# Optimization experiments

Hardware: AMD Instinct MI355X
Metric: run time of the kernel (lower is better)

## Reference

```python
import jax, jax.numpy as jnp
import numpy as np
import math

B, S, D, H, DFF = 4, 1024, 1024, 16, 4096
DH = D // H
ALPHA = 1.0
NEG = -1e20
EPS = 1e-5


def layernorm(x, g, b):
    mu = jnp.mean(x, axis=-1, keepdims=True)
    var = jnp.mean((x - mu) ** 2, axis=-1, keepdims=True)
    return (x - mu) * jax.lax.rsqrt(var + EPS) * g + b


def setup_inputs() -> dict:
    key = jax.random.key(0)
    ks = jax.random.split(key, 16)
    sc = 1.0 / math.sqrt(D)
    inp = {
        "x": jax.random.normal(ks[0], (B, S, D), jnp.float32),
        "mask": jnp.ones((B, 1, S), jnp.float32),
        "Wq": jax.random.normal(ks[1], (D, D), jnp.float32) * sc,
        "Wk": jax.random.normal(ks[2], (D, D), jnp.float32) * sc,
        "Wv": jax.random.normal(ks[3], (D, D), jnp.float32) * sc,
        "ln1_g": jnp.ones((DH,), jnp.float32),
        "ln1_b": jnp.zeros((DH,), jnp.float32),
        "Wo": jax.random.normal(ks[4], (D, D), jnp.float32) * sc,
        "bo": jnp.zeros((D,), jnp.float32),
        "ln2_g": jnp.ones((D,), jnp.float32),
        "ln2_b": jnp.zeros((D,), jnp.float32),
        "Ws": jax.random.normal(ks[5], (D, D), jnp.float32) * sc,
        "Wh": jax.random.normal(ks[6], (D, D), jnp.float32) * sc,
        "b_f": jnp.zeros((D,), jnp.float32),
        "lnfg_g": jnp.ones((D,), jnp.float32),
        "lnfg_b": jnp.zeros((D,), jnp.float32),
        "Wp1": jax.random.normal(ks[7], (DFF, D), jnp.float32) * sc,
        "bp1": jnp.zeros((DFF,), jnp.float32),
        "Wp2": jax.random.normal(ks[8], (D, DFF), jnp.float32) / math.sqrt(DFF),
        "bp2": jnp.zeros((D,), jnp.float32),
        "lnffn_g": jnp.ones((D,), jnp.float32),
        "lnffn_b": jnp.zeros((D,), jnp.float32),
    }
    return inp


def reference(x, mask, Wq, Wk, Wv, ln1_g, ln1_b, Wo, bo, ln2_g, ln2_b,
              Ws, Wh, b_f, lnfg_g, lnfg_b, Wp1, bp1, Wp2, bp2, lnffn_g, lnffn_b):
    b, s, d = x.shape
    # --- masked multi-head attention ---
    q = (x @ Wq.T).reshape(b, s, H, DH)
    k = (x @ Wk.T).reshape(b, s, H, DH)
    v = (x @ Wv.T).reshape(b, s, H, DH)
    q = layernorm(q, ln1_g, ln1_b)
    k = layernorm(k, ln1_g, ln1_b)
    v = layernorm(v, ln1_g, ln1_b)
    energy = jnp.einsum('nqhd,nkhd->nhqk', q, k)  # (B,H,S,S)
    # directional mask: forward pass -> strictly lower triangular allowed (0), else -1e20
    idx = jnp.arange(s)
    allowed = idx[:, None] > idx[None, :]  # tril(diagonal=-1)
    dir_mask = jnp.where(allowed, 0.0, NEG).astype(x.dtype)  # (S,S)
    m = jnp.broadcast_to(mask, (b, H, s))  # (B,H,S)
    pair = m[:, :, :, None] * m[:, :, None, :]  # (B,H,S,S)
    final_mask = pair * dir_mask[None, None]
    dist_mask = -jnp.abs(idx[:, None] - idx[None, :]).astype(x.dtype)  # (S,S)
    pre = energy / math.sqrt(d) + final_mask + ALPHA * dist_mask[None, None]
    attn = jax.nn.softmax(pre, axis=-1)
    # faithful to source einsum 'nhql,nlhd->nlhd' (sums attention over q)
    out = jnp.einsum('nhql,nlhd->nlhd', attn, v)
    out = out.reshape(b, s, d)
    out = out @ Wo.T + bo
    h = layernorm(out, ln2_g, ln2_b)
    # --- fusion gate and norm ---
    s_f = layernorm(x @ Ws.T, lnfg_g, lnfg_b)
    h_f = layernorm(h @ Wh.T, lnfg_g, lnfg_b)
    f = jax.nn.sigmoid(s_f + h_f + b_f)
    g = layernorm(f * s_f + (1.0 - f) * h_f, lnfg_g, lnfg_b)
    # --- position-wise FFN + residual + norm ---
    ff = jax.nn.relu(g @ Wp1.T + bp1) @ Wp2.T + bp2
    return layernorm(ff + g, lnffn_g, lnffn_b)
```

## Files before the change

kernel.cpp:

```cpp
#include <hip/hip_runtime.h>

constexpr int CB   = 4;
constexpr int CS   = 1024;
constexpr int CD   = 1024;
constexpr int CH   = 16;
constexpr int CDFF = 4096;
constexpr int CNT  = CB * CS;

typedef unsigned short ush;
typedef __bf16 bf16_t;
typedef bf16_t bf16x8 __attribute__((ext_vector_type(8)));
typedef float  f32x4  __attribute__((ext_vector_type(4)));

__device__ __forceinline__ ush f2bf(float f) {
    union { float f; unsigned u; } v; v.f = f;
    unsigned u = v.u;
    return (ush)((u + 0x7fffu + ((u >> 16) & 1u)) >> 16);
}
__device__ __forceinline__ float bf2f(ush h) {
    union { unsigned u; float f; } v; v.u = ((unsigned)h) << 16;
    return v.f;
}
__device__ __forceinline__ void ub8(uint4 v, float* d) {
    d[0] = bf2f((ush)v.x); d[1] = bf2f((ush)(v.x >> 16));
    d[2] = bf2f((ush)v.y); d[3] = bf2f((ush)(v.y >> 16));
    d[4] = bf2f((ush)v.z); d[5] = bf2f((ush)(v.z >> 16));
    d[6] = bf2f((ush)v.w); d[7] = bf2f((ush)(v.w >> 16));
}
__device__ __forceinline__ uint4 pb8(const float* d) {
    uint4 v;
    v.x = (unsigned)f2bf(d[0]) | ((unsigned)f2bf(d[1]) << 16);
    v.y = (unsigned)f2bf(d[2]) | ((unsigned)f2bf(d[3]) << 16);
    v.z = (unsigned)f2bf(d[4]) | ((unsigned)f2bf(d[5]) << 16);
    v.w = (unsigned)f2bf(d[6]) | ((unsigned)f2bf(d[7]) << 16);
    return v;
}

__device__ __forceinline__ void gll16(const void* g, void* l) {
    __builtin_amdgcn_global_load_lds((const __attribute__((address_space(1))) void*)g,
                                     (__attribute__((address_space(3))) void*)l,
                                     16, 0, 0);
}

constexpr int Q4 = (CD * CD) / 4;
__global__ __launch_bounds__(256) void k_convert_all(
        const float4* __restrict__ Wq, const float4* __restrict__ Wk,
        const float4* __restrict__ Wv, const float4* __restrict__ Ws,
        const float4* __restrict__ Wo, const float4* __restrict__ Wh,
        const float4* __restrict__ Wp1, const float4* __restrict__ Wp2,
        const float4* __restrict__ x, uint4* __restrict__ arena,
        uint4* __restrict__ xb, float4* __restrict__ wz) {
    int i = blockIdx.x * 256 + threadIdx.x;
    int stride = gridDim.x * 256;
    for (int i2 = i; i2 < (CB * CH * CS) / 4; i2 += stride)
        wz[i2] = (float4){0.f, 0.f, 0.f, 0.f};
    for (; i < 9 * Q4; i += stride) {
        const int F = i * 2;
        const int seg = F >> 18;
        const float4* src; int off;
        if (seg < 6) {
            src = (seg == 0) ? Wq : (seg == 1) ? Wk : (seg == 2) ? Wv
                : (seg == 3) ? Ws : (seg == 4) ? Wo : Wh;
            off = F & (Q4 - 1);
        } else if (seg < 10) { src = Wp1; off = F - 6 * Q4; }
        else if (seg < 14)   { src = Wp2; off = F - 10 * Q4; }
        else                 { src = x;   off = F - 14 * Q4; }
        float4 a = src[off], b = src[off + 1];
        uint4 o;
        o.x = (unsigned)f2bf(a.x) | ((unsigned)f2bf(a.y) << 16);
        o.y = (unsigned)f2bf(a.z) | ((unsigned)f2bf(a.w) << 16);
        o.z = (unsigned)f2bf(b.x) | ((unsigned)f2bf(b.y) << 16);
        o.w = (unsigned)f2bf(b.z) | ((unsigned)f2bf(b.w) << 16);
        if (seg < 14) arena[i] = o;
        else          xb[i - 7 * Q4] = o;
    }
}

template <int TN, int EPI, int SPLITK>
__global__ __launch_bounds__(256, 4) void k_gemm_bt(
        const ush* __restrict__ A, const ush* __restrict__ Bm,
        ush* __restrict__ Cb,
        const float* __restrict__ bias, const float* __restrict__ bias2,
        ush* __restrict__ out2, ush* __restrict__ out3, ush* __restrict__ sb,
        int N, int K) {
    constexpr int NJ  = TN / 32;
    constexpr int BCH = TN / 32;
    constexpr int EPS = TN + 8;
    constexpr int STG = (128 + TN) * 64;
    constexpr int LDS_USH = (STG > 128 * EPS) ? STG : 128 * EPS;
    __shared__ ush smem[LDS_USH];
    ush* As = smem;
    ush* Bs = smem + 128 * 64;
    ush* Cs = smem;

    const int tid  = threadIdx.x;
    const int wave = tid >> 6, lane = tid & 63;
    const int quad = lane >> 4, r = lane & 15;
    const int wm = wave >> 1, wn = wave & 1;
    const int bm = blockIdx.x, bn = blockIdx.y;

    const int kcnt  = K / SPLITK;
    const int kbase = blockIdx.z * kcnt;
    ush* dst0 = Cb;
    if (SPLITK > 1) dst0 += (size_t)blockIdx.z * (size_t)gridDim.x * 128 * N;

    const int trow = tid >> 3, tk8 = tid & 7;
    const int kcl  = tk8 ^ (trow & 7);
    const ush* ap = A  + (size_t)(bm * 128 + trow) * K + kbase + kcl * 8;
    const ush* bp = Bm + (size_t)(bn * TN  + trow) * K + kbase + kcl * 8;
    ush* asd = As + tid * 8;
    ush* bsd = Bs + tid * 8;
    const size_t cstep = (size_t)32 * K;

    f32x4 acc[4][NJ];
#pragma unroll
    for (int i = 0; i < 4; i++)
#pragma unroll
        for (int j = 0; j < NJ; j++) acc[i][j] = (f32x4){0.f, 0.f, 0.f, 0.f};

    const int rx = r & 7;
    for (int k0 = 0; k0 < kcnt; k0 += 64) {
#pragma unroll
        for (int c = 0; c < 4; c++)   gll16(ap + c * cstep, asd + c * 2048);
#pragma unroll
        for (int c = 0; c < BCH; c++) gll16(bp + c * cstep, bsd + c * 2048);
        ap += 64; bp += 64;
        __syncthreads();
#pragma unroll
        for (int h = 0; h < 2; h++) {
            const int kx = (((h << 2) | quad) ^ rx) * 8;
            bf16x8 af[4], bfv[NJ];
#pragma unroll
            for (int i = 0; i < 4; i++)
                af[i] = *(const bf16x8*)(As + (wm * 64 + i * 16 + r) * 64 + kx);
#pragma unroll
            for (int j = 0; j < NJ; j++)
                bfv[j] = *(const bf16x8*)(Bs + (wn * (TN / 2) + j * 16 + r) * 64 + kx);
#pragma unroll
            for (int i = 0; i < 4; i++)
#pragma unroll
                for (int j = 0; j < NJ; j++)
                    acc[i][j] = __builtin_amdgcn_mfma_f32_16x16x32_bf16(af[i], bfv[j], acc[i][j], 0, 0, 0);
        }
        __syncthreads();
    }

    if (EPI == 4 && bn < 24) {
        float g4[4], b4[4];
#pragma unroll
        for (int j = 0; j < 4; j++) { g4[j] = bias[j * 16 + r]; b4[j] = bias2[j * 16 + r]; }
#pragma unroll
        for (int i = 0; i < 4; i++) {
            const int row = wm * 64 + i * 16 + quad * 4;
#pragma unroll
            for (int g = 0; g < 4; g++) {
                float s = 0.f, q = 0.f;
#pragma unroll
                for (int j = 0; j < 4; j++) { float v = acc[i][j][g]; s += v; q += v * v; }
                s += __shfl_xor(s, 1); q += __shfl_xor(q, 1);
                s += __shfl_xor(s, 2); q += __shfl_xor(q, 2);
                s += __shfl_xor(s, 4); q += __shfl_xor(q, 4);
                s += __shfl_xor(s, 8); q += __shfl_xor(q, 8);
                float mu   = s * (1.f / 64.f);
                float rstd = rsqrtf(q * (1.f / 64.f) - mu * mu + 1e-5f);
#pragma unroll
                for (int j = 0; j < 4; j++) {
                    float y = (acc[i][j][g] - mu) * rstd * g4[j] + b4[j];
                    Cs[(row + g) * EPS + wn * 64 + j * 16 + r] = f2bf(y);
                }
            }
        }
    } else {
#pragma unroll
        for (int i = 0; i < 4; i++) {
            const int row = wm * 64 + i * 16 + quad * 4;
#pragma unroll
            for (int j = 0; j < NJ; j++) {
                const int col = wn * (TN / 2) + j * 16 + r;
                float bv = (EPI == 3) ? bias[bn * TN + col] : 0.f;
#pragma unroll
                for (int g = 0; g < 4; g++) {
                    float v = acc[i][j][g] + bv;
                    if (EPI == 3) v = fmaxf(v, 0.f);
                    Cs[(row + g) * EPS + col] = f2bf(v);
                }
            }
        }
    }
    __syncthreads();

    ush* dst = dst0;
    int colbase = bn * TN, Nn = N;
    if (EPI == 4) {
        Nn = 1024;
        if (bn < 8)       { dst = Cb;   colbase = bn * 128; }
        else if (bn < 16) { dst = out2; colbase = (bn - 8) * 128; }
        else if (bn < 24) { dst = out3; colbase = (bn - 16) * 128; }
        else              { dst = sb;   colbase = (bn - 24) * 128; }
    }
    const int tpr = TN / 8;
    const int rpp = 2048 / TN;
    const int srow2 = tid / tpr;
    const int scol2 = (tid % tpr) * 8;
#pragma unroll
    for (int pp = 0; pp < TN / 16; pp++) {
        const int rr = pp * rpp + srow2;
        uint4 vv = *(const uint4*)&Cs[rr * EPS + scol2];
        *(uint4*)&dst[(size_t)(bm * 128 + rr) * Nn + colbase + scol2] = vv;
    }
}

__global__ __launch_bounds__(256) void k_attn(const ush* __restrict__ qb,
                                              const ush* __restrict__ kb,
                                              const float* __restrict__ mask,
                                              float* __restrict__ wcol) {
    __shared__ ush   Qs[64][72];
    __shared__ ush   Ks[64][72];
    __shared__ float colpart[4][64];

    const int tid  = threadIdx.x;
    const int wave = tid >> 6, lane = tid & 63;
    const int quad = lane >> 4, r = lane & 15;
    const int bh = blockIdx.x, bi = bh >> 4, hi = bh & 15;
    const int q0 = blockIdx.y * 64;

    {
        int row = tid >> 2, seg = (tid & 3) * 16;
        const ush* src = qb + ((size_t)(bi * CS + q0 + row) * CD + hi * 64 + seg);
        *(uint4*)&Qs[row][seg]     = *(const uint4*)src;
        *(uint4*)&Qs[row][seg + 8] = *(const uint4*)(src + 8);
    }
    __syncthreads();
    bf16x8 af0 = *(const bf16x8*)&Qs[wave * 16 + r][quad * 8];
    bf16x8 af1 = *(const bf16x8*)&Qs[wave * 16 + r][32 + quad * 8];

    float mq[4];
#pragma unroll
    for (int g = 0; g < 4; g++) mq[g] = mask[bi * CS + q0 + wave * 16 + quad * 4 + g];

    const int t0 = (q0 >= 128) ? 0 : ((q0 >= 64) ? 1 : 2);
    float pr[3][4][4];
    float s_loc[4] = {0.f, 0.f, 0.f, 0.f};

    for (int t = t0; t < 3; t++) {
        const int l0 = q0 - 128 + t * 64;
        __syncthreads();
        {
            int row = tid >> 2, seg = (tid & 3) * 16;
            const ush* src = kb + ((size_t)(bi * CS + l0 + row) * CD + hi * 64 + seg);
            *(uint4*)&Ks[row][seg]     = *(const uint4*)src;
            *(uint4*)&Ks[row][seg + 8] = *(const uint4*)(src + 8);
        }
        __syncthreads();
#pragma unroll
        for (int jt = 0; jt < 4; jt++) {
            bf16x8 bf0 = *(const bf16x8*)&Ks[jt * 16 + r][quad * 8];
            bf16x8 bf1 = *(const bf16x8*)&Ks[jt * 16 + r][32 + quad * 8];
            f32x4 sc = (f32x4){0.f, 0.f, 0.f, 0.f};
            sc = __builtin_amdgcn_mfma_f32_16x16x32_bf16(af0, bf0, sc, 0, 0, 0);
            sc = __builtin_amdgcn_mfma_f32_16x16x32_bf16(af1, bf1, sc, 0, 0, 0);
            const int l = l0 + jt * 16 + r;
            const float ml = mask[bi * CS + l];
#pragma unroll
            for (int g = 0; g < 4; g++) {
                const int qg = q0 + wave * 16 + quad * 4 + g;
                float e  = sc[g] * 0.03125f;
                float mv = (qg > l) ? 0.f : mq[g] * ml * (-1e20f);
                float p  = __expf(e + mv - fabsf((float)(qg - l)) - 8.f);
                pr[t][jt][g] = p;
                s_loc[g] += p;
            }
        }
    }

    float rs[4];
#pragma unroll
    for (int g = 0; g < 4; g++) {
        float s = s_loc[g];
        s += __shfl_xor(s, 1); s += __shfl_xor(s, 2);
        s += __shfl_xor(s, 4); s += __shfl_xor(s, 8);
        rs[g] = (s > 0.f) ? 1.f / s : 0.f;
    }

    for (int t = t0; t < 3; t++) {
        const int l0 = q0 - 128 + t * 64;
#pragma unroll
        for (int jt = 0; jt < 4; jt++) {
            float csum = 0.f;
#pragma unroll
            for (int g = 0; g < 4; g++) csum += pr[t][jt][g] * rs[g];
            csum += __shfl_xor(csum, 16);
            csum += __shfl_xor(csum, 32);
            if (quad == 0) colpart[wave][jt * 16 + r] = csum;
        }
        __syncthreads();
        if (tid < 64) {
            float v = colpart[0][tid] + colpart[1][tid] + colpart[2][tid] + colpart[3][tid];
            atomicAdd(&wcol[(size_t)bh * CS + l0 + tid], v);
        }
        __syncthreads();
    }
}

__global__ __launch_bounds__(256) void k_scale_v(const ush* __restrict__ vb,
                                                 const float* __restrict__ wcol,
                                                 ush* __restrict__ out) {
    const int g = blockIdx.x * 256 + threadIdx.x;
    const int token = g >> 7;
    const int cg = g & 127;
    const int c0 = cg * 8, h = cg >> 3;
    const int l = token & (CS - 1), b = token >> 10;
    const float w = wcol[(size_t)(b * CH + h) * CS + l] + (1.f / 1024.f);
    float d[8];
    ub8(*(const uint4*)&vb[(size_t)token * CD + c0], d);
#pragma unroll
    for (int j = 0; j < 8; j++) d[j] *= w;
    *(uint4*)&out[(size_t)token * CD + c0] = pb8(d);
}

__device__ __forceinline__ void stats128(float s, float q, float* red,
                                         int wave, int lane, float& mu, float& rstd) {
#pragma unroll
    for (int off = 32; off >= 1; off >>= 1) {
        s += __shfl_xor(s, off);
        q += __shfl_xor(q, off);
    }
    if (lane == 0) { red[wave] = s; red[2 + wave] = q; }
    __syncthreads();
    s = red[0] + red[1];
    q = red[2] + red[3];
    mu = s * (1.f / 1024.f);
    rstd = rsqrtf(q * (1.f / 1024.f) - mu * mu + 1e-5f);
    __syncthreads();
}

template <int MODE>
__global__ __launch_bounds__(128) void k_ln_row(const ush* __restrict__ b0,
                                                const ush* __restrict__ b1,
                                                const ush* __restrict__ b2,
                                                const float* __restrict__ badd,
                                                const float* __restrict__ gam,
                                                const float* __restrict__ bet,
                                                float* __restrict__ outf,
                                                ush* __restrict__ outb) {
    __shared__ float red[4];
    const int tid = threadIdx.x, wave = tid >> 6, lane = tid & 63;
    const size_t base = (size_t)blockIdx.x * CD;
    const int c0 = tid * 8;
    float t[8], sr[8], tmp[8], gv[8], bv[8];
    float s = 0.f, q = 0.f, mu, rstd;

    *(float4*)&gv[0] = *(const float4*)&gam[c0];
    *(float4*)&gv[4] = *(const float4*)&gam[c0 + 4];
    *(float4*)&bv[0] = *(const float4*)&bet[c0];
    *(float4*)&bv[4] = *(const float4*)&bet[c0 + 4];

    if (MODE == 2) {
        float av[8];
        *(float4*)&av[0] = *(const float4*)&badd[c0];
        *(float4*)&av[4] = *(const float4*)&badd[c0 + 4];
        ub8(*(const uint4*)&b0[base + c0], sr);
        ub8(*(const uint4*)&b1[base + c0], t);
        ub8(*(const uint4*)&b2[base + c0], tmp);
#pragma unroll
        for (int j = 0; j < 8; j++) t[j] += tmp[j];
#pragma unroll
        for (int j = 0; j < 8; j++) { s += sr[j]; q += sr[j] * sr[j]; }
        stats128(s, q, red, wave, lane, mu, rstd);
#pragma unroll
        for (int j = 0; j < 8; j++) sr[j] = (sr[j] - mu) * rstd * gv[j] + bv[j];
        s = 0.f; q = 0.f;
#pragma unroll
        for (int j = 0; j < 8; j++) { s += t[j]; q += t[j] * t[j]; }
        stats128(s, q, red, wave, lane, mu, rstd);
#pragma unroll
        for (int j = 0; j < 8; j++) {
            float hf = (t[j] - mu) * rstd * gv[j] + bv[j];
            float f  = 1.f / (1.f + __expf(-(sr[j] + hf + av[j])));
            t[j] = f * sr[j] + (1.f - f) * hf;
        }
    } else {
        float av[8];
        *(float4*)&av[0] = *(const float4*)&badd[c0];
        *(float4*)&av[4] = *(const float4*)&badd[c0 + 4];
        ub8(*(const uint4*)&b0[base + c0], t);
        ub8(*(const uint4*)&b1[base + c0], tmp);
#pragma unroll
        for (int j = 0; j < 8; j++) t[j] += tmp[j] + av[j];
        if (MODE == 3) {
            ub8(*(const uint4*)&b2[base + c0], tmp);
#pragma unroll
            for (int j = 0; j < 8; j++) t[j] += tmp[j];
        }
    }

    s = 0.f; q = 0.f;
#pragma unroll
    for (int j = 0; j < 8; j++) { s += t[j]; q += t[j] * t[j]; }
    stats128(s, q, red, wave, lane, mu, rstd);

    float y[8];
#pragma unroll
    for (int j = 0; j < 8; j++) y[j] = (t[j] - mu) * rstd * gv[j] + bv[j];
    if (MODE == 3) {
        *(float4*)&outf[base + c0]     = *(float4*)&y[0];
        *(float4*)&outf[base + c0 + 4] = *(float4*)&y[4];
    } else {
        *(uint4*)&outb[base + c0] = pb8(y);
    }
}

extern "C" void kernel_launch(void* const* d_in, const int* in_sizes, int n_in,
                              void* d_out, int out_size, void* d_ws, size_t ws_size,
                              hipStream_t stream) {
    const float* x    = (const float*)d_in[0];
    const float* mask = (const float*)d_in[1];
    const float* Wq   = (const float*)d_in[2];
    const float* Wk   = (const float*)d_in[3];
    const float* Wv   = (const float*)d_in[4];
    const float* ln1g = (const float*)d_in[5];
    const float* ln1b = (const float*)d_in[6];
    const float* Wo   = (const float*)d_in[7];
    const float* bo   = (const float*)d_in[8];
    const float* ln2g = (const float*)d_in[9];
    const float* ln2b = (const float*)d_in[10];
    const float* Ws   = (const float*)d_in[11];
    const float* Wh   = (const float*)d_in[12];
    const float* bf_  = (const float*)d_in[13];
    const float* lnfgg = (const float*)d_in[14];
    const float* lnfgb = (const float*)d_in[15];
    const float* Wp1  = (const float*)d_in[16];
    const float* bp1  = (const float*)d_in[17];
    const float* Wp2  = (const float*)d_in[18];
    const float* bp2  = (const float*)d_in[19];
    const float* lnffg = (const float*)d_in[20];
    const float* lnffb = (const float*)d_in[21];
    float* out = (float*)d_out;

    char* p = (char*)d_ws;
    auto alloc = [&](size_t bytes) -> char* {
        char* r = p;
        p += (bytes + 255) & ~(size_t)255;
        return r;
    };
    ush*   arena = (ush*)alloc((size_t)14 * CD * CD * 2);
    ush*   Wob   = arena + (size_t)4 * CD * CD;
    ush*   Whb   = arena + (size_t)5 * CD * CD;
    ush*   Wp1b  = arena + (size_t)6 * CD * CD;
    ush*   Wp2b  = arena + (size_t)10 * CD * CD;
    ush*   xb    = (ush*)alloc((size_t)CNT * CD * 2);
    ush*   klnb  = (ush*)alloc((size_t)CNT * CD * 2);
    ush*   vb    = (ush*)alloc((size_t)CNT * CD * 2);
    ush*   qlnb  = (ush*)alloc((size_t)CNT * CD * 2);
    ush*   gb    = (ush*)alloc((size_t)CNT * CD * 2);
    ush*   P     = (ush*)alloc((size_t)2 * CNT * CD * 2);
    ush*   P1    = P + (size_t)CNT * CD;
    ush*   ff1b  = (ush*)alloc((size_t)CNT * CDFF * 2);
    float* wcol  = (float*)alloc((size_t)CB * CH * CS * 4);
    ush*   sbuf  = ff1b;
    ush*   attb  = qlnb;
    ush*   hb    = klnb;

    dim3 blk(256);

    k_convert_all<<<dim3(4608), blk, 0, stream>>>(
        (const float4*)Wq, (const float4*)Wk, (const float4*)Wv, (const float4*)Ws,
        (const float4*)Wo, (const float4*)Wh, (const float4*)Wp1, (const float4*)Wp2,
        (const float4*)x, (uint4*)arena, (uint4*)xb, (float4*)wcol);

    k_gemm_bt<128, 4, 1><<<dim3(32, 32, 1), blk, 0, stream>>>(
        xb, arena, qlnb, ln1g, ln1b, klnb, vb, sbuf, 4096, CD);

    k_attn<<<dim3(CB * CH, CS / 64), blk, 0, stream>>>(qlnb, klnb, mask, wcol);
    k_scale_v<<<dim3(CNT * CD / 8 / 256), blk, 0, stream>>>(vb, wcol, attb);

    k_gemm_bt<64, 0, 2><<<dim3(32, 16, 2), blk, 0, stream>>>(
        attb, Wob, P, nullptr, nullptr, nullptr, nullptr, nullptr, CD, CD);
    k_ln_row<0><<<dim3(CNT), dim3(128), 0, stream>>>(P, P1, nullptr, bo, ln2g, ln2b, nullptr, hb);

    k_gemm_bt<64, 0, 2><<<dim3(32, 16, 2), blk, 0, stream>>>(
        hb, Whb, P, nullptr, nullptr, nullptr, nullptr, nullptr, CD, CD);
    k_ln_row<2><<<dim3(CNT), dim3(128), 0, stream>>>(sbuf, P, P1, bf_, lnfgg, lnfgb, nullptr, gb);

    k_gemm_bt<128, 3, 1><<<dim3(32, 32, 1), blk, 0, stream>>>(
        gb, Wp1b, ff1b, bp1, nullptr, nullptr, nullptr, nullptr, CDFF, CD);
    k_gemm_bt<64, 0, 2><<<dim3(32, 16, 2), blk, 0, stream>>>(
        ff1b, Wp2b, P, nullptr, nullptr, nullptr, nullptr, nullptr, CD, CDFF);
    k_ln_row<3><<<dim3(CNT), dim3(128), 0, stream>>>(P, P1, gb, bp2, lnffg, lnffb, out, nullptr);

    (void)in_sizes; (void)n_in; (void)out_size; (void)ws_size;
}
```

Baseline: 347.5 us.

## Replace GEMM with 4-stage async pipelined 512-thread kernel, drop split-K

Replaces the single-buffered 256-thread bf16 GEMM with a 512-thread, 128x128-tile kernel that keeps a four-slot LDS ring fed by direct global-to-LDS loads three tiles ahead. It uses explicit vmcnt waits and raw barriers instead of two syncthreads per K step, and raises wave priority around the MFMA block. Split-K for the N=1024 GEMMs is removed, so the layernorm kernels no longer read and add a second partial buffer. The intent is to hide global-load latency and cut partial-sum traffic. The cost is a 128 KB LDS footprint that allows one block per CU, and fewer blocks for the N=1024 GEMMs.

```diff
diff --git a/kernel.cpp b/kernel.cpp
--- a/kernel.cpp
+++ b/kernel.cpp
@@ -76,82 +76,88 @@
     }
 }
 
-template <int TN, int EPI, int SPLITK>
-__global__ __launch_bounds__(256, 4) void k_gemm_bt(
+template <int EPI>
+__global__ __launch_bounds__(512) void k_gemm_p4(
         const ush* __restrict__ A, const ush* __restrict__ Bm,
         ush* __restrict__ Cb,
         const float* __restrict__ bias, const float* __restrict__ bias2,
         ush* __restrict__ out2, ush* __restrict__ out3, ush* __restrict__ sb,
         int N, int K) {
-    constexpr int NJ  = TN / 32;
-    constexpr int BCH = TN / 32;
-    constexpr int EPS = TN + 8;
-    constexpr int STG = (128 + TN) * 64;
-    constexpr int LDS_USH = (STG > 128 * EPS) ? STG : 128 * EPS;
-    __shared__ ush smem[LDS_USH];
-    ush* As = smem;
-    ush* Bs = smem + 128 * 64;
-    ush* Cs = smem;
+    __shared__ ush sm[4 * 16384];
 
     const int tid  = threadIdx.x;
     const int wave = tid >> 6, lane = tid & 63;
     const int quad = lane >> 4, r = lane & 15;
     const int wm = wave >> 1, wn = wave & 1;
     const int bm = blockIdx.x, bn = blockIdx.y;
-
-    const int kcnt  = K / SPLITK;
-    const int kbase = blockIdx.z * kcnt;
-    ush* dst0 = Cb;
-    if (SPLITK > 1) dst0 += (size_t)blockIdx.z * (size_t)gridDim.x * 128 * N;
+    const int NT = K >> 6;
 
     const int trow = tid >> 3, tk8 = tid & 7;
     const int kcl  = tk8 ^ (trow & 7);
-    const ush* ap = A  + (size_t)(bm * 128 + trow) * K + kbase + kcl * 8;
-    const ush* bp = Bm + (size_t)(bn * TN  + trow) * K + kbase + kcl * 8;
-    ush* asd = As + tid * 8;
-    ush* bsd = Bs + tid * 8;
-    const size_t cstep = (size_t)32 * K;
-
-    f32x4 acc[4][NJ];
-#pragma unroll
-    for (int i = 0; i < 4; i++)
-#pragma unroll
-        for (int j = 0; j < NJ; j++) acc[i][j] = (f32x4){0.f, 0.f, 0.f, 0.f};
+    const ush* ap = A  + (size_t)(bm * 128 + trow) * K + kcl * 8;
+    const ush* bp = Bm + (size_t)(bn * 128 + trow) * K + kcl * 8;
+
+    f32x4 acc[2][4];
+#pragma unroll
+    for (int i = 0; i < 2; i++)
+#pragma unroll
+        for (int j = 0; j < 4; j++) acc[i][j] = (f32x4){0.f, 0.f, 0.f, 0.f};
+
+    auto STAGE = [&](int tt) {
+        ush* sl = sm + (tt & 3) * 16384;
+        const ush* aq = ap + tt * 64;
+        const ush* bq = bp + tt * 64;
+        gll16(aq,                  sl + tid * 8);
+        gll16(aq + (size_t)64 * K, sl + 4096  + tid * 8);
+        gll16(bq,                  sl + 8192  + tid * 8);
+        gll16(bq + (size_t)64 * K, sl + 12288 + tid * 8);
+    };
+
+    STAGE(0); STAGE(1); STAGE(2);
+    asm volatile("s_waitcnt vmcnt(8)" ::: "memory");
+    __builtin_amdgcn_s_barrier();
 
     const int rx = r & 7;
-    for (int k0 = 0; k0 < kcnt; k0 += 64) {
-#pragma unroll
-        for (int c = 0; c < 4; c++)   gll16(ap + c * cstep, asd + c * 2048);
-#pragma unroll
-        for (int c = 0; c < BCH; c++) gll16(bp + c * cstep, bsd + c * 2048);
-        ap += 64; bp += 64;
-        __syncthreads();
-#pragma unroll
-        for (int h = 0; h < 2; h++) {
+    for (int t = 0; t < NT; ++t) {
+        if (t + 3 < NT) STAGE(t + 3);
+        const ush* sA = sm + (t & 3) * 16384;
+        const ush* sB = sA + 8192;
+        __builtin_amdgcn_s_setprio(1);
+#pragma unroll
+        for (int h = 0; h < 2; ++h) {
             const int kx = (((h << 2) | quad) ^ rx) * 8;
-            bf16x8 af[4], bfv[NJ];
-#pragma unroll
-            for (int i = 0; i < 4; i++)
-                af[i] = *(const bf16x8*)(As + (wm * 64 + i * 16 + r) * 64 + kx);
-#pragma unroll
-            for (int j = 0; j < NJ; j++)
-                bfv[j] = *(const bf16x8*)(Bs + (wn * (TN / 2) + j * 16 + r) * 64 + kx);
-#pragma unroll
-            for (int i = 0; i < 4; i++)
-#pragma unroll
-                for (int j = 0; j < NJ; j++)
+            bf16x8 af[2], bfv[4];
+#pragma unroll
+            for (int i = 0; i < 2; i++)
+                af[i] = *(const bf16x8*)(sA + (wm * 32 + i * 16 + r) * 64 + kx);
+#pragma unroll
+            for (int j = 0; j < 4; j++)
+                bfv[j] = *(const bf16x8*)(sB + (wn * 64 + j * 16 + r) * 64 + kx);
+#pragma unroll
+            for (int i = 0; i < 2; i++)
+#pragma unroll
+                for (int j = 0; j < 4; j++)
                     acc[i][j] = __builtin_amdgcn_mfma_f32_16x16x32_bf16(af[i], bfv[j], acc[i][j], 0, 0, 0);
         }
-        __syncthreads();
-    }
-
-    if (EPI == 4 && bn < 24) {
+        __builtin_amdgcn_s_setprio(0);
+        const int rem = NT - 1 - t;
+        if (rem >= 3)      asm volatile("s_waitcnt vmcnt(8)" ::: "memory");
+        else if (rem == 2) asm volatile("s_waitcnt vmcnt(4)" ::: "memory");
+        else if (rem == 1) asm volatile("s_waitcnt vmcnt(0)" ::: "memory");
+        if (rem) __builtin_amdgcn_s_barrier();
+    }
+
+    __syncthreads();
+    constexpr int EPS2 = 136;
+    ush* Cs = sm;
+
+    if (EPI == 4 && (bn >> 3) < 3) {
         float g4[4], b4[4];
 #pragma unroll
         for (int j = 0; j < 4; j++) { g4[j] = bias[j * 16 + r]; b4[j] = bias2[j * 16 + r]; }
 #pragma unroll
-        for (int i = 0; i < 4; i++) {
-            const int row = wm * 64 + i * 16 + quad * 4;
+        for (int i = 0; i < 2; i++) {
+            const int row = wm * 32 + i * 16 + quad * 4;
 #pragma unroll
             for (int g = 0; g < 4; g++) {
                 float s = 0.f, q = 0.f;
@@ -166,47 +172,42 @@
 #pragma unroll
                 for (int j = 0; j < 4; j++) {
                     float y = (acc[i][j][g] - mu) * rstd * g4[j] + b4[j];
-                    Cs[(row + g) * EPS + wn * 64 + j * 16 + r] = f2bf(y);
+                    Cs[(row + g) * EPS2 + wn * 64 + j * 16 + r] = f2bf(y);
                 }
             }
         }
     } else {
 #pragma unroll
-        for (int i = 0; i < 4; i++) {
-            const int row = wm * 64 + i * 16 + quad * 4;
-#pragma unroll
-            for (int j = 0; j < NJ; j++) {
-                const int col = wn * (TN / 2) + j * 16 + r;
-                float bv = (EPI == 3) ? bias[bn * TN + col] : 0.f;
+        for (int i = 0; i < 2; i++) {
+            const int row = wm * 32 + i * 16 + quad * 4;
+#pragma unroll
+            for (int j = 0; j < 4; j++) {
+                const int col = wn * 64 + j * 16 + r;
+                float bv = (EPI == 3) ? bias[bn * 128 + col] : 0.f;
 #pragma unroll
                 for (int g = 0; g < 4; g++) {
                     float v = acc[i][j][g] + bv;
                     if (EPI == 3) v = fmaxf(v, 0.f);
-                    Cs[(row + g) * EPS + col] = f2bf(v);
+                    Cs[(row + g) * EPS2 + col] = f2bf(v);
                 }
             }
         }
     }
     __syncthreads();
 
-    ush* dst = dst0;
-    int colbase = bn * TN, Nn = N;
+    ush* dst = Cb; int colbase = bn * 128, Nn = N;
     if (EPI == 4) {
         Nn = 1024;
-        if (bn < 8)       { dst = Cb;   colbase = bn * 128; }
-        else if (bn < 16) { dst = out2; colbase = (bn - 8) * 128; }
-        else if (bn < 24) { dst = out3; colbase = (bn - 16) * 128; }
-        else              { dst = sb;   colbase = (bn - 24) * 128; }
-    }
-    const int tpr = TN / 8;
-    const int rpp = 2048 / TN;
-    const int srow2 = tid / tpr;
-    const int scol2 = (tid % tpr) * 8;
-#pragma unroll
-    for (int pp = 0; pp < TN / 16; pp++) {
-        const int rr = pp * rpp + srow2;
-        uint4 vv = *(const uint4*)&Cs[rr * EPS + scol2];
-        *(uint4*)&dst[(size_t)(bm * 128 + rr) * Nn + colbase + scol2] = vv;
+        const int quarter = bn >> 3;
+        colbase = (bn & 7) * 128;
+        dst = (quarter == 0) ? Cb : (quarter == 1) ? out2 : (quarter == 2) ? out3 : sb;
+    }
+#pragma unroll
+    for (int p = 0; p < 4; p++) {
+        const int rr = p * 32 + (tid >> 4);
+        const int cc = (tid & 15) * 8;
+        uint4 vv = *(const uint4*)&Cs[rr * EPS2 + cc];
+        *(uint4*)&dst[(size_t)(bm * 128 + rr) * Nn + colbase + cc] = vv;
     }
 }
 
@@ -361,9 +362,6 @@
         *(float4*)&av[4] = *(const float4*)&badd[c0 + 4];
         ub8(*(const uint4*)&b0[base + c0], sr);
         ub8(*(const uint4*)&b1[base + c0], t);
-        ub8(*(const uint4*)&b2[base + c0], tmp);
-#pragma unroll
-        for (int j = 0; j < 8; j++) t[j] += tmp[j];
 #pragma unroll
         for (int j = 0; j < 8; j++) { s += sr[j]; q += sr[j] * sr[j]; }
         stats128(s, q, red, wave, lane, mu, rstd);
@@ -384,9 +382,8 @@
         *(float4*)&av[0] = *(const float4*)&badd[c0];
         *(float4*)&av[4] = *(const float4*)&badd[c0 + 4];
         ub8(*(const uint4*)&b0[base + c0], t);
-        ub8(*(const uint4*)&b1[base + c0], tmp);
-#pragma unroll
-        for (int j = 0; j < 8; j++) t[j] += tmp[j] + av[j];
+#pragma unroll
+        for (int j = 0; j < 8; j++) t[j] += av[j];
         if (MODE == 3) {
             ub8(*(const uint4*)&b2[base + c0], tmp);
 #pragma unroll
@@ -462,31 +459,32 @@
     ush*   hb    = klnb;
 
     dim3 blk(256);
+    dim3 gblk(512);
 
     k_convert_all<<<dim3(4608), blk, 0, stream>>>(
         (const float4*)Wq, (const float4*)Wk, (const float4*)Wv, (const float4*)Ws,
         (const float4*)Wo, (const float4*)Wh, (const float4*)Wp1, (const float4*)Wp2,
         (const float4*)x, (uint4*)arena, (uint4*)xb, (float4*)wcol);
 
-    k_gemm_bt<128, 4, 1><<<dim3(32, 32, 1), blk, 0, stream>>>(
+    k_gemm_p4<4><<<dim3(32, 32), gblk, 0, stream>>>(
         xb, arena, qlnb, ln1g, ln1b, klnb, vb, sbuf, 4096, CD);
 
     k_attn<<<dim3(CB * CH, CS / 64), blk, 0, stream>>>(qlnb, klnb, mask, wcol);
     k_scale_v<<<dim3(CNT * CD / 8 / 256), blk, 0, stream>>>(vb, wcol, attb);
 
-    k_gemm_bt<64, 0, 2><<<dim3(32, 16, 2), blk, 0, stream>>>(
+    k_gemm_p4<0><<<dim3(32, 8), gblk, 0, stream>>>(
         attb, Wob, P, nullptr, nullptr, nullptr, nullptr, nullptr, CD, CD);
-    k_ln_row<0><<<dim3(CNT), dim3(128), 0, stream>>>(P, P1, nullptr, bo, ln2g, ln2b, nullptr, hb);
-
-    k_gemm_bt<64, 0, 2><<<dim3(32, 16, 2), blk, 0, stream>>>(
-        hb, Whb, P, nullptr, nullptr, nullptr, nullptr, nullptr, CD, CD);
-    k_ln_row<2><<<dim3(CNT), dim3(128), 0, stream>>>(sbuf, P, P1, bf_, lnfgg, lnfgb, nullptr, gb);
-
-    k_gemm_bt<128, 3, 1><<<dim3(32, 32, 1), blk, 0, stream>>>(
+    k_ln_row<0><<<dim3(CNT), dim3(128), 0, stream>>>(P, nullptr, nullptr, bo, ln2g, ln2b, nullptr, hb);
+
+    k_gemm_p4<0><<<dim3(32, 8), gblk, 0, stream>>>(
+        hb, Whb, P1, nullptr, nullptr, nullptr, nullptr, nullptr, CD, CD);
+    k_ln_row<2><<<dim3(CNT), dim3(128), 0, stream>>>(sbuf, P1, nullptr, bf_, lnfgg, lnfgb, nullptr, gb);
+
+    k_gemm_p4<3><<<dim3(32, 32), gblk, 0, stream>>>(
         gb, Wp1b, ff1b, bp1, nullptr, nullptr, nullptr, nullptr, CDFF, CD);
-    k_gemm_bt<64, 0, 2><<<dim3(32, 16, 2), blk, 0, stream>>>(
+    k_gemm_p4<0><<<dim3(32, 8), gblk, 0, stream>>>(
         ff1b, Wp2b, P, nullptr, nullptr, nullptr, nullptr, nullptr, CD, CDFF);
-    k_ln_row<3><<<dim3(CNT), dim3(128), 0, stream>>>(P, P1, gb, bp2, lnffg, lnffb, out, nullptr);
+    k_ln_row<3><<<dim3(CNT), dim3(128), 0, stream>>>(P, nullptr, gb, bp2, lnffg, lnffb, out, nullptr);
 
     (void)in_sizes; (void)n_in; (void)out_size; (void)ws_size;
 }
```

After: 368.5 us. 1.06x slower.

## Add 256x256 eight-wave GEMM kernel with phased LDS pipeline for large projections

Applied to the files above, without the earlier changes.

Adds a new 512-thread GEMM kernel with 256x256 output tiles, double-buffered direct-to-LDS loads and a phase-interleaved load/MFMA schedule with priority hints. It is used for the fused QKV/Ws projection (with the per-head layernorm epilogue), the FFN up-projection, and the FFN down-projection, which now uses split-K of 4 with partial sums written into the weight arena. The final layernorm kernel sums the four partials. The intent is more operand reuse per LDS load and better overlap of loads with compute, at the cost of higher register and LDS pressure and an extra partial-sum pass.

```diff
diff --git a/kernel.cpp b/kernel.cpp
--- a/kernel.cpp
+++ b/kernel.cpp
@@ -6,6 +6,7 @@
 constexpr int CH   = 16;
 constexpr int CDFF = 4096;
 constexpr int CNT  = CB * CS;
+constexpr size_t SZE = (size_t)CNT * CD;
 
 typedef unsigned short ush;
 typedef __bf16 bf16_t;
@@ -76,6 +77,184 @@
     }
 }
 
+template <int EPI, int SPLITK>
+__global__ __launch_bounds__(512, 2) void k_gemm8(
+        const ush* __restrict__ A, const ush* __restrict__ Bm,
+        ush* __restrict__ Cb,
+        const float* __restrict__ bias, const float* __restrict__ bias2,
+        ush* __restrict__ out2, ush* __restrict__ out3, ush* __restrict__ sb,
+        int N, int K) {
+    __shared__ ush sm[2 * 32768];
+
+    const int tid  = threadIdx.x;
+    const int wave = tid >> 6, lane = tid & 63;
+    const int quad = lane >> 4, r = lane & 15;
+    const int wm = wave >> 2, wn = wave & 3;
+    const int bm = blockIdx.x, bn = blockIdx.y;
+    const int kcnt = K / SPLITK, kbase = blockIdx.z * kcnt;
+    const int NT = kcnt >> 6;
+
+    ush* dst0 = Cb;
+    if (SPLITK > 1)
+        dst0 = ((blockIdx.z < 2) ? Cb : out2)
+             + (size_t)(blockIdx.z & 1) * (size_t)gridDim.x * 256 * N;
+
+    const int trow = tid >> 3, tk8 = tid & 7;
+    const int kcl  = tk8 ^ (trow & 7);
+    const ush* ap = A  + (size_t)(bm * 256 + trow) * K + kbase + kcl * 8;
+    const ush* bp = Bm + (size_t)(bn * 256 + trow) * K + kbase + kcl * 8;
+
+    f32x4 acc[8][4];
+#pragma unroll
+    for (int i = 0; i < 8; i++)
+#pragma unroll
+        for (int j = 0; j < 4; j++) acc[i][j] = (f32x4){0.f, 0.f, 0.f, 0.f};
+
+    auto SH = [&](int mat, int hf, int tt) {
+        const ush* src = (mat ? bp : ap) + tt * 64 + (size_t)(hf * 128) * K;
+        ush* d = sm + (tt & 1) * 32768 + mat * 16384 + hf * 8192 + tid * 8;
+        gll16(src,                  d);
+        gll16(src + (size_t)64 * K, d + 4096);
+    };
+
+    SH(0, 0, 0); SH(0, 1, 0); SH(1, 0, 0); SH(1, 1, 0);
+    SH(0, 0, 1); SH(1, 1, 1);
+    asm volatile("s_waitcnt vmcnt(4)" ::: "memory");
+    __builtin_amdgcn_s_barrier();
+
+    const ush* s1b = sm + 32768;
+    for (int t = 0; t < NT; t += 2) {
+        const bool s2 = (t + 2) < NT, s3 = (t + 3) < NT;
+        bf16x8 a[4][2], b0r[2][2], b1r[2][2];
+
+        auto RA = [&](int ah, const ush* sl) {
+#pragma unroll
+            for (int i = 0; i < 4; i++)
+#pragma unroll
+                for (int h = 0; h < 2; h++) {
+                    const int row = wm * 128 + ah * 64 + i * 16 + r;
+                    a[i][h] = *(const bf16x8*)(sl + row * 64 + ((((h << 2) | quad) ^ (row & 7)) << 3));
+                }
+        };
+        auto RB = [&](bf16x8 (&bq)[2][2], int bh, const ush* sl) {
+#pragma unroll
+            for (int j = 0; j < 2; j++)
+#pragma unroll
+                for (int h = 0; h < 2; h++) {
+                    const int row = wn * 64 + bh * 32 + j * 16 + r;
+                    bq[j][h] = *(const bf16x8*)(sl + 16384 + row * 64 + ((((h << 2) | quad) ^ (row & 7)) << 3));
+                }
+        };
+        auto MM = [&](bf16x8 (&bq)[2][2], int ai, int bj) {
+            __builtin_amdgcn_s_setprio(1);
+#pragma unroll
+            for (int i = 0; i < 4; i++)
+#pragma unroll
+                for (int j = 0; j < 2; j++)
+#pragma unroll
+                    for (int h = 0; h < 2; h++)
+                        acc[ai + i][bj + j] =
+                            __builtin_amdgcn_mfma_f32_16x16x32_bf16(a[i][h], bq[j][h], acc[ai + i][bj + j], 0, 0, 0);
+            __builtin_amdgcn_s_setprio(0);
+        };
+#define PH_SYNC  __builtin_amdgcn_s_barrier();                         \
+                 asm volatile("s_waitcnt lgkmcnt(0)" ::: "memory");    \
+                 __builtin_amdgcn_sched_barrier(0);
+
+        RA(0, sm); RB(b0r, 0, sm);  SH(0, 1, t + 1);
+        PH_SYNC; MM(b0r, 0, 0); __builtin_amdgcn_s_barrier();
+        RB(b1r, 1, sm);             SH(1, 0, t + 1);
+        PH_SYNC; MM(b1r, 0, 2); __builtin_amdgcn_s_barrier();
+        RA(1, sm);                  if (s2) SH(0, 0, t + 2);
+        PH_SYNC; MM(b1r, 4, 2); __builtin_amdgcn_s_barrier();
+        if (s2) SH(1, 1, t + 2);
+        MM(b0r, 4, 0);
+        if (s2) asm volatile("s_waitcnt vmcnt(4)" ::: "memory");
+        else    asm volatile("s_waitcnt vmcnt(0)" ::: "memory");
+        __builtin_amdgcn_s_barrier();
+
+        RA(0, s1b); RB(b0r, 0, s1b); if (s2) SH(0, 1, t + 2);
+        PH_SYNC; MM(b0r, 0, 0); __builtin_amdgcn_s_barrier();
+        RB(b1r, 1, s1b);             if (s2) SH(1, 0, t + 2);
+        PH_SYNC; MM(b1r, 0, 2); __builtin_amdgcn_s_barrier();
+        RA(1, s1b);                  if (s3) SH(0, 0, t + 3);
+        PH_SYNC; MM(b1r, 4, 2); __builtin_amdgcn_s_barrier();
+        if (s3) SH(1, 1, t + 3);
+        MM(b0r, 4, 0);
+        if (s3) asm volatile("s_waitcnt vmcnt(4)" ::: "memory");
+        else    asm volatile("s_waitcnt vmcnt(0)" ::: "memory");
+        __builtin_amdgcn_s_barrier();
+#undef PH_SYNC
+    }
+    asm volatile("s_waitcnt vmcnt(0)" ::: "memory");
+    __syncthreads();
+
+    constexpr int EPS2 = 264;
+    ush* Cs = sm;
+#pragma unroll
+    for (int hh = 0; hh < 2; hh++) {
+        if (wm == hh) {
+            if (EPI == 4 && bn < 12) {
+                float g4[4], b4[4];
+#pragma unroll
+                for (int j = 0; j < 4; j++) { g4[j] = bias[j * 16 + r]; b4[j] = bias2[j * 16 + r]; }
+#pragma unroll
+                for (int i = 0; i < 8; i++) {
+                    const int row = i * 16 + quad * 4;
+#pragma unroll
+                    for (int g = 0; g < 4; g++) {
+                        float s = 0.f, q = 0.f;
+#pragma unroll
+                        for (int j = 0; j < 4; j++) { float v = acc[i][j][g]; s += v; q += v * v; }
+                        s += __shfl_xor(s, 1); q += __shfl_xor(q, 1);
+                        s += __shfl_xor(s, 2); q += __shfl_xor(q, 2);
+                        s += __shfl_xor(s, 4); q += __shfl_xor(q, 4);
+                        s += __shfl_xor(s, 8); q += __shfl_xor(q, 8);
+                        float mu   = s * (1.f / 64.f);
+                        float rstd = rsqrtf(q * (1.f / 64.f) - mu * mu + 1e-5f);
+#pragma unroll
+                        for (int j = 0; j < 4; j++) {
+                            float y = (acc[i][j][g] - mu) * rstd * g4[j] + b4[j];
+                            Cs[(row + g) * EPS2 + wn * 64 + j * 16 + r] = f2bf(y);
+                        }
+                    }
+                }
+            } else {
+#pragma unroll
+                for (int i = 0; i < 8; i++) {
+#pragma unroll
+                    for (int j = 0; j < 4; j++) {
+                        const int col = wn * 64 + j * 16 + r;
+                        float bv = (EPI == 3) ? bias[bn * 256 + col] : 0.f;
+#pragma unroll
+                        for (int g = 0; g < 4; g++) {
+                            float v = acc[i][j][g] + bv;
+                            if (EPI == 3) v = fmaxf(v, 0.f);
+                            Cs[(i * 16 + quad * 4 + g) * EPS2 + col] = f2bf(v);
+                        }
+                    }
+                }
+            }
+        }
+        __syncthreads();
+        ush* dst = dst0; int colbase = bn * 256, Nn = N;
+        if (EPI == 4) {
+            Nn = 1024;
+            const int quarter = bn >> 2;
+            colbase = (bn & 3) * 256;
+            dst = (quarter == 0) ? Cb : (quarter == 1) ? out2 : (quarter == 2) ? out3 : sb;
+        }
+#pragma unroll
+        for (int p2 = 0; p2 < 8; p2++) {
+            const int rr = p2 * 16 + (tid >> 5);
+            const int cc = (tid & 31) * 8;
+            uint4 vv = *(const uint4*)&Cs[rr * EPS2 + cc];
+            *(uint4*)&dst[(size_t)(bm * 256 + hh * 128 + rr) * Nn + colbase + cc] = vv;
+        }
+        __syncthreads();
+    }
+}
+
 template <int TN, int EPI, int SPLITK>
 __global__ __launch_bounds__(256, 4) void k_gemm_bt(
         const ush* __restrict__ A, const ush* __restrict__ Bm,
@@ -145,59 +324,23 @@
         __syncthreads();
     }
 
-    if (EPI == 4 && bn < 24) {
-        float g4[4], b4[4];
-#pragma unroll
-        for (int j = 0; j < 4; j++) { g4[j] = bias[j * 16 + r]; b4[j] = bias2[j * 16 + r]; }
-#pragma unroll
-        for (int i = 0; i < 4; i++) {
-            const int row = wm * 64 + i * 16 + quad * 4;
+#pragma unroll
+    for (int i = 0; i < 4; i++) {
+        const int row = wm * 64 + i * 16 + quad * 4;
+#pragma unroll
+        for (int j = 0; j < NJ; j++) {
+            const int col = wn * (TN / 2) + j * 16 + r;
+            float bv = (EPI == 3) ? bias[bn * TN + col] : 0.f;
 #pragma unroll
             for (int g = 0; g < 4; g++) {
-                float s = 0.f, q = 0.f;
-#pragma unroll
-                for (int j = 0; j < 4; j++) { float v = acc[i][j][g]; s += v; q += v * v; }
-                s += __shfl_xor(s, 1); q += __shfl_xor(q, 1);
-                s += __shfl_xor(s, 2); q += __shfl_xor(q, 2);
-                s += __shfl_xor(s, 4); q += __shfl_xor(q, 4);
-                s += __shfl_xor(s, 8); q += __shfl_xor(q, 8);
-                float mu   = s * (1.f / 64.f);
-                float rstd = rsqrtf(q * (1.f / 64.f) - mu * mu + 1e-5f);
-#pragma unroll
-                for (int j = 0; j < 4; j++) {
-                    float y = (acc[i][j][g] - mu) * rstd * g4[j] + b4[j];
-                    Cs[(row + g) * EPS + wn * 64 + j * 16 + r] = f2bf(y);
-                }
+                float v = acc[i][j][g] + bv;
+                if (EPI == 3) v = fmaxf(v, 0.f);
+                Cs[(row + g) * EPS + col] = f2bf(v);
             }
         }
-    } else {
-#pragma unroll
-        for (int i = 0; i < 4; i++) {
-            const int row = wm * 64 + i * 16 + quad * 4;
-#pragma unroll
-            for (int j = 0; j < NJ; j++) {
-                const int col = wn * (TN / 2) + j * 16 + r;
-                float bv = (EPI == 3) ? bias[bn * TN + col] : 0.f;
-#pragma unroll
-                for (int g = 0; g < 4; g++) {
-                    float v = acc[i][j][g] + bv;
-                    if (EPI == 3) v = fmaxf(v, 0.f);
-                    Cs[(row + g) * EPS + col] = f2bf(v);
-                }
-            }
-        }
     }
     __syncthreads();
 
-    ush* dst = dst0;
-    int colbase = bn * TN, Nn = N;
-    if (EPI == 4) {
-        Nn = 1024;
-        if (bn < 8)       { dst = Cb;   colbase = bn * 128; }
-        else if (bn < 16) { dst = out2; colbase = (bn - 8) * 128; }
-        else if (bn < 24) { dst = out3; colbase = (bn - 16) * 128; }
-        else              { dst = sb;   colbase = (bn - 24) * 128; }
-    }
     const int tpr = TN / 8;
     const int rpp = 2048 / TN;
     const int srow2 = tid / tpr;
@@ -206,7 +349,7 @@
     for (int pp = 0; pp < TN / 16; pp++) {
         const int rr = pp * rpp + srow2;
         uint4 vv = *(const uint4*)&Cs[rr * EPS + scol2];
-        *(uint4*)&dst[(size_t)(bm * 128 + rr) * Nn + colbase + scol2] = vv;
+        *(uint4*)&dst0[(size_t)(bm * 128 + rr) * N + bn * TN + scol2] = vv;
     }
 }
 
@@ -379,6 +522,25 @@
             float f  = 1.f / (1.f + __expf(-(sr[j] + hf + av[j])));
             t[j] = f * sr[j] + (1.f - f) * hf;
         }
+    } else if (MODE == 3) {
+        float av[8];
+        *(float4*)&av[0] = *(const float4*)&badd[c0];
+        *(float4*)&av[4] = *(const float4*)&badd[c0 + 4];
+        ub8(*(const uint4*)&b0[base + c0], t);
+#pragma unroll
+        for (int j = 0; j < 8; j++) t[j] += av[j];
+        ub8(*(const uint4*)&b0[base + SZE + c0], tmp);
+#pragma unroll
+        for (int j = 0; j < 8; j++) t[j] += tmp[j];
+        ub8(*(const uint4*)&b1[base + c0], tmp);
+#pragma unroll
+        for (int j = 0; j < 8; j++) t[j] += tmp[j];
+        ub8(*(const uint4*)&b1[base + SZE + c0], tmp);
+#pragma unroll
+        for (int j = 0; j < 8; j++) t[j] += tmp[j];
+        ub8(*(const uint4*)&b2[base + c0], tmp);
+#pragma unroll
+        for (int j = 0; j < 8; j++) t[j] += tmp[j];
     } else {
         float av[8];
         *(float4*)&av[0] = *(const float4*)&badd[c0];
@@ -387,11 +549,6 @@
         ub8(*(const uint4*)&b1[base + c0], tmp);
 #pragma unroll
         for (int j = 0; j < 8; j++) t[j] += tmp[j] + av[j];
-        if (MODE == 3) {
-            ub8(*(const uint4*)&b2[base + c0], tmp);
-#pragma unroll
-            for (int j = 0; j < 8; j++) t[j] += tmp[j];
-        }
     }
 
     s = 0.f; q = 0.f;
@@ -454,21 +611,23 @@
     ush*   qlnb  = (ush*)alloc((size_t)CNT * CD * 2);
     ush*   gb    = (ush*)alloc((size_t)CNT * CD * 2);
     ush*   P     = (ush*)alloc((size_t)2 * CNT * CD * 2);
-    ush*   P1    = P + (size_t)CNT * CD;
+    ush*   P1    = P + SZE;
     ush*   ff1b  = (ush*)alloc((size_t)CNT * CDFF * 2);
     float* wcol  = (float*)alloc((size_t)CB * CH * CS * 4);
     ush*   sbuf  = ff1b;
     ush*   attb  = qlnb;
     ush*   hb    = klnb;
+    ush*   P23   = arena;
 
     dim3 blk(256);
+    dim3 gblk(512);
 
     k_convert_all<<<dim3(4608), blk, 0, stream>>>(
         (const float4*)Wq, (const float4*)Wk, (const float4*)Wv, (const float4*)Ws,
         (const float4*)Wo, (const float4*)Wh, (const float4*)Wp1, (const float4*)Wp2,
         (const float4*)x, (uint4*)arena, (uint4*)xb, (float4*)wcol);
 
-    k_gemm_bt<128, 4, 1><<<dim3(32, 32, 1), blk, 0, stream>>>(
+    k_gemm8<4, 1><<<dim3(16, 16, 1), gblk, 0, stream>>>(
         xb, arena, qlnb, ln1g, ln1b, klnb, vb, sbuf, 4096, CD);
 
     k_attn<<<dim3(CB * CH, CS / 64), blk, 0, stream>>>(qlnb, klnb, mask, wcol);
@@ -482,11 +641,11 @@
         hb, Whb, P, nullptr, nullptr, nullptr, nullptr, nullptr, CD, CD);
     k_ln_row<2><<<dim3(CNT), dim3(128), 0, stream>>>(sbuf, P, P1, bf_, lnfgg, lnfgb, nullptr, gb);
 
-    k_gemm_bt<128, 3, 1><<<dim3(32, 32, 1), blk, 0, stream>>>(
+    k_gemm8<3, 1><<<dim3(16, 16, 1), gblk, 0, stream>>>(
         gb, Wp1b, ff1b, bp1, nullptr, nullptr, nullptr, nullptr, CDFF, CD);
-    k_gemm_bt<64, 0, 2><<<dim3(32, 16, 2), blk, 0, stream>>>(
-        ff1b, Wp2b, P, nullptr, nullptr, nullptr, nullptr, nullptr, CD, CDFF);
-    k_ln_row<3><<<dim3(CNT), dim3(128), 0, stream>>>(P, P1, gb, bp2, lnffg, lnffb, out, nullptr);
+    k_gemm8<0, 4><<<dim3(16, 4, 4), gblk, 0, stream>>>(
+        ff1b, Wp2b, P, nullptr, nullptr, P23, nullptr, nullptr, CD, CDFF);
+    k_ln_row<3><<<dim3(CNT), dim3(128), 0, stream>>>(P, P23, gb, bp2, lnffg, lnffb, out, nullptr);
 
     (void)in_sizes; (void)n_in; (void)out_size; (void)ws_size;
 }
```

Result: slower. 366.2 us (+5.4%).
